# Optimization experiments

Measured on AMD Instinct MI355X. Metric: run time of the kernel, lower is better.

The kernel has to match this reference:

```python
import jax, jax.numpy as jnp
import numpy as np


def setup_inputs() -> dict:
    key = jax.random.key(0)
    k1, k2, k3, k4 = jax.random.split(key, 4)
    B, T, E, D = 4, 4096, 2048, 128
    x = jax.random.normal(k1, (B, T, E), dtype=jnp.float32)
    # nn.Linear(E, D, bias=False): y = x @ W where W is [E, D]
    scale = 1.0 / np.sqrt(E)
    Wq = jax.random.normal(k2, (E, D), dtype=jnp.float32) * scale
    Wk = jax.random.normal(k3, (E, D), dtype=jnp.float32) * scale
    Wv = jax.random.normal(k4, (E, D), dtype=jnp.float32) * scale
    return {"x": x, "Wq": Wq, "Wk": Wk, "Wv": Wv}


def reference(x, Wq, Wk, Wv):
    # Single attention head, prefill path (kv_cache=None, T_q == T_k).
    D = Wq.shape[1]
    Q = jnp.einsum('bte,ed->btd', x, Wq)
    K = jnp.einsum('bte,ed->btd', x, Wk)
    V = jnp.einsum('bte,ed->btd', x, Wv)
    scores = jnp.einsum('bqd,bkd->bqk', Q, K) / jnp.sqrt(jnp.float32(D))
    T = x.shape[1]
    causal = jnp.tril(jnp.ones((T, T), dtype=bool))  # [T_q, T_k]
    scores = jnp.where(causal[None, :, :], scores, -jnp.inf)
    attn = jax.nn.softmax(scores, axis=-1)
    out = jnp.einsum('bqk,bkd->bqd', attn, V)
    return out
```

## Files before the change

kernel.cpp:

```cpp
#include <hip/hip_runtime.h>
#include <hip/hip_bf16.h>

typedef short bf16x8 __attribute__((ext_vector_type(8)));
typedef float f32x4  __attribute__((ext_vector_type(4)));

#define T_SEQ 4096
#define NB    4
#define E_DIM 2048
#define D_DIM 128
#define M_TOT (NB * T_SEQ)
#define NCHUNK 4
#define CHUNK_KT 16
#define SM_SHIFT 12.0f

__device__ __forceinline__ ushort f2bf(float f) {
  union { float f; unsigned u; } c; c.f = f;
  unsigned u = c.u;
  unsigned r = (u + 0x7FFFu + ((u >> 16) & 1u)) >> 16;
  return (ushort)r;
}
__device__ __forceinline__ float bf2f(ushort u) {
  union { unsigned u; float f; } c; c.u = ((unsigned)u) << 16;
  return c.f;
}
__device__ __forceinline__ bf16x8 cvt8(const float4& lo, const float4& hi) {
  union { __hip_bfloat162 h; ushort u[2]; } t;
  union { ushort u[8]; bf16x8 v; } r;
  t.h = __float22bfloat162_rn(make_float2(lo.x, lo.y)); r.u[0] = t.u[0]; r.u[1] = t.u[1];
  t.h = __float22bfloat162_rn(make_float2(lo.z, lo.w)); r.u[2] = t.u[0]; r.u[3] = t.u[1];
  t.h = __float22bfloat162_rn(make_float2(hi.x, hi.y)); r.u[4] = t.u[0]; r.u[5] = t.u[1];
  t.h = __float22bfloat162_rn(make_float2(hi.z, hi.w)); r.u[6] = t.u[0]; r.u[7] = t.u[1];
  return r.v;
}

__device__ __forceinline__ void gl2lds16(const void* g, void* l) {
  __builtin_amdgcn_global_load_lds(
      (const __attribute__((address_space(1))) unsigned int*)g,
      (__attribute__((address_space(3))) unsigned int*)l, 16, 0, 0);
}

__global__ __launch_bounds__(256) void build_wt(const float* __restrict__ Wq,
                                                const float* __restrict__ Wk,
                                                const float* __restrict__ Wv,
                                                ushort* __restrict__ Wt) {
  __shared__ ushort tile[64][72];
  const int tid = threadIdx.x;
  const int k0 = blockIdx.x * 64, n0 = blockIdx.y * 64, o = blockIdx.z;
  const float* W = (o == 0) ? Wq : ((o == 1) ? Wk : Wv);
  for (int i = 0; i < 4; i++) {
    int c = tid + i * 256;
    int r = c >> 4, c4 = (c & 15) * 4;
    float4 v = *(const float4*)(W + (size_t)(k0 + r) * D_DIM + n0 + c4);
    ushort4 b4;
    b4.x = f2bf(v.x); b4.y = f2bf(v.y); b4.z = f2bf(v.z); b4.w = f2bf(v.w);
    *(ushort4*)(&tile[r][c4]) = b4;
  }
  __syncthreads();
  for (int i = 0; i < 2; i++) {
    int c = tid + i * 256;
    int nn = c >> 3, k8 = (c & 7) * 8;
    ushort tmp[8];
    for (int j = 0; j < 8; j++) tmp[j] = tile[k8 + j][nn];
    *(uint4*)(Wt + (size_t)((o << 7) + n0 + nn) * E_DIM + k0 + k8) = *(const uint4*)tmp;
  }
}

__global__ __launch_bounds__(256, 4) void qkv_gemm(const float* __restrict__ x,
                                                   const ushort* __restrict__ Wt,
                                                   ushort* __restrict__ Q,
                                                   ushort* __restrict__ K,
                                                   ushort* __restrict__ V) {
  __shared__ ushort As[2][64 * 64];
  __shared__ ushort Bs[2][96 * 64];

  const int tid  = threadIdx.x;
  const int wave = tid >> 6, lane = tid & 63;
  const int quad = lane >> 4, l16 = lane & 15;
  const int wm = wave >> 1, wn = wave & 1;
  const int m0 = blockIdx.x * 64;
  const int n0 = blockIdx.y * 96;

  f32x4 acc[2][3] = {};

  const int s_ = wave * 64 + lane;
  const int n_ = s_ >> 3, p_ = s_ & 7;

  const int ar_ = tid >> 2, aq4_ = tid & 3;
  const float* xrow = x + (size_t)(m0 + ar_) * E_DIM + aq4_ * 16;

#define DMA_B(k0_, buf_)                                                        \
  _Pragma("unroll")                                                             \
  for (int i_ = 0; i_ < 3; i_++) {                                              \
    int slotbase = i_ * 256 + wave * 64;                                        \
    int n = (i_ * 32) + n_;                           \
    int cg = p_ ^ (n & 7);                                                      \
    gl2lds16(Wt + (size_t)(n0 + n) * E_DIM + (k0_) + cg * 8,                    \
             (char*)(buf_) + (size_t)slotbase * 16);                            \
  }

#define GLOAD_A(k0_)                                                            \
  {                                                                             \
    const float* ap_ = xrow + (k0_);                                            \
    areg0 = *(const float4*)(ap_);                                              \
    areg1 = *(const float4*)(ap_ + 4);                                          \
    areg2 = *(const float4*)(ap_ + 8);                                          \
    areg3 = *(const float4*)(ap_ + 12);                                         \
  }

#define CVT_WRITE_A(bufidx)                                                     \
  {                                                                             \
    ushort* as_ = As[bufidx];                                                   \
    bf16x8 w0_ = cvt8(areg0, areg1);                                            \
    bf16x8 w1_ = cvt8(areg2, areg3);                                            \
    *(bf16x8*)(as_ + ar_ * 64 + (((aq4_ * 2)     ^ (ar_ & 7)) * 8)) = w0_;      \
    *(bf16x8*)(as_ + ar_ * 64 + (((aq4_ * 2 + 1) ^ (ar_ & 7)) * 8)) = w1_;      \
  }

#define COMPUTE(bufidx)                                                         \
  {                                                                             \
    const ushort* as_ = As[bufidx];                                             \
    const ushort* bs_ = Bs[bufidx];                                             \
    _Pragma("unroll")                                                           \
    for (int kk = 0; kk < 2; kk++) {                                            \
      const int slot = ((kk * 4 + quad) ^ (l16 & 7)) * 8;                       \
      bf16x8 af0 = *(const bf16x8*)(as_ + (wm * 32 + l16) * 64 + slot);         \
      bf16x8 af1 = *(const bf16x8*)(as_ + (wm * 32 + 16 + l16) * 64 + slot);    \
      _Pragma("unroll")                                                         \
      for (int ni = 0; ni < 3; ni++) {                                          \
        int n = wn * 48 + ni * 16 + l16;                                        \
        bf16x8 bf = *(const bf16x8*)(bs_ + n * 64 + slot);                      \
        acc[0][ni] = __builtin_amdgcn_mfma_f32_16x16x32_bf16(af0, bf, acc[0][ni], 0, 0, 0); \
        acc[1][ni] = __builtin_amdgcn_mfma_f32_16x16x32_bf16(af1, bf, acc[1][ni], 0, 0, 0); \
      }                                                                         \
    }                                                                           \
  }

  float4 areg0, areg1, areg2, areg3;

  GLOAD_A(0);
  DMA_B(0, Bs[0]);
  CVT_WRITE_A(0);
  __syncthreads();

  for (int it = 0; it < 32; it += 2) {
    GLOAD_A((it + 1) * 64);
    DMA_B((it + 1) * 64, Bs[1]);
    COMPUTE(0);
    CVT_WRITE_A(1);
    __syncthreads();
    if (it < 30) {
      GLOAD_A((it + 2) * 64);
      DMA_B((it + 2) * 64, Bs[0]);
      COMPUTE(1);
      CVT_WRITE_A(0);
      __syncthreads();
    } else {
      COMPUTE(1);
    }
  }

  for (int mi = 0; mi < 2; mi++)
    for (int ni = 0; ni < 3; ni++) {
      int colall = n0 + wn * 48 + ni * 16 + l16;
      int o = colall >> 7, d = colall & 127;
      ushort* dst = (o == 0) ? Q : ((o == 1) ? K : V);
      for (int r = 0; r < 4; r++) {
        int row = m0 + wm * 32 + mi * 16 + quad * 4 + r;
        dst[(size_t)row * D_DIM + d] = f2bf(acc[mi][ni][r]);
      }
    }
#undef DMA_B
#undef GLOAD_A
#undef CVT_WRITE_A
#undef COMPUTE
}

__global__ __launch_bounds__(256) void v_transpose(const ushort* __restrict__ V,
                                                   ushort* __restrict__ Vt) {
  __shared__ ushort tile[64][72];
  const int tid = threadIdx.x;
  const int t0 = blockIdx.x * 64, d0 = blockIdx.y * 64, b = blockIdx.z;
  for (int i = 0; i < 2; i++) {
    int c = tid + i * 256;
    int r = c >> 3, cc = (c & 7) * 8;
    *(uint4*)(&tile[r][cc]) = *(const uint4*)(V + (size_t)(b * T_SEQ + t0 + r) * D_DIM + d0 + cc);
  }
  __syncthreads();
  for (int i = 0; i < 2; i++) {
    int c = tid + i * 256;
    int dr = c >> 3, tc = (c & 7) * 8;
    ushort tmp[8];
    for (int j = 0; j < 8; j++) tmp[j] = tile[tc + j][dr];
    *(uint4*)(Vt + (size_t)(b * D_DIM + d0 + dr) * T_SEQ + t0 + tc) = *(const uint4*)tmp;
  }
}

__global__ __launch_bounds__(256) void attn_partial(const ushort* __restrict__ Q,
                                                    const ushort* __restrict__ K,
                                                    const ushort* __restrict__ Vt,
                                                    ushort* __restrict__ Po,
                                                    float* __restrict__ Ll) {
  const int qt = blockIdx.x, cq = blockIdx.y, b = blockIdx.z;
  const int kt0 = cq * CHUNK_KT;
  if (kt0 > qt) return;

  __shared__ ushort Kt[64][136];
  __shared__ ushort Vts[128][72];
  __shared__ ushort Pls[4][16][72];

  const int tid = threadIdx.x;
  const int wave = tid >> 6, lane = tid & 63;
  const int quad = lane >> 4, l16 = lane & 15;

  const int qrow = qt * 64 + wave * 16 + l16;
  bf16x8 qf[4];
  for (int kk = 0; kk < 4; kk++)
    qf[kk] = *(const bf16x8*)(Q + (size_t)(b * T_SEQ + qrow) * D_DIM + kk * 32 + quad * 8);

  bf16x8 ones;
  for (int j = 0; j < 8; j++) ones[j] = (short)0x3F80;

  f32x4 o_acc[8] = {};
  f32x4 lacc = {};
  const float scale2 = 0.08838834764831845f * 1.4426950408889634f;

  const int kt1 = min(qt, kt0 + CHUNK_KT - 1);

  for (int kt = kt0; kt <= kt1; kt++) {
    __syncthreads();
    for (int i = 0; i < 4; i++) {
      int c = tid + i * 256;
      int r = c >> 4, col = (c & 15) * 8;
      *(uint4*)(&Kt[r][col]) = *(const uint4*)(K + (size_t)(b * T_SEQ + kt * 64 + r) * D_DIM + col);
    }
    for (int i = 0; i < 4; i++) {
      int c = tid + i * 256;
      int dr = c >> 3, col = (c & 7) * 8;
      *(uint4*)(&Vts[dr][col]) = *(const uint4*)(Vt + (size_t)(b * D_DIM + dr) * T_SEQ + kt * 64 + col);
    }
    __syncthreads();

    f32x4 s[4] = {};
    for (int kk = 0; kk < 4; kk++) {
      const int kc = kk * 32 + quad * 8;
      for (int ni = 0; ni < 4; ni++) {
        bf16x8 bf = *(const bf16x8*)(&Kt[ni * 16 + l16][kc]);
        s[ni] = __builtin_amdgcn_mfma_f32_16x16x32_bf16(qf[kk], bf, s[ni], 0, 0, 0);
      }
    }
    if (kt == qt) {
      for (int ni = 0; ni < 4; ni++) {
        int kidx = kt * 64 + ni * 16 + l16;
        for (int r = 0; r < 4; r++) {
          int qidx = qt * 64 + wave * 16 + quad * 4 + r;
          float v = (kidx > qidx) ? -1e30f : (s[ni][r] * scale2 - SM_SHIFT);
          s[ni][r] = exp2f(v);
        }
      }
    } else {
      for (int ni = 0; ni < 4; ni++)
        for (int r = 0; r < 4; r++)
          s[ni][r] = exp2f(s[ni][r] * scale2 - SM_SHIFT);
    }
    for (int ni = 0; ni < 4; ni++)
      for (int r = 0; r < 4; r++)
        Pls[wave][quad * 4 + r][ni * 16 + l16] = f2bf(s[ni][r]);
    for (int kk2 = 0; kk2 < 2; kk2++) {
      const int kc = kk2 * 32 + quad * 8;
      bf16x8 pf = *(const bf16x8*)(&Pls[wave][l16][kc]);
      for (int ni = 0; ni < 8; ni++) {
        bf16x8 vf = *(const bf16x8*)(&Vts[ni * 16 + l16][kc]);
        o_acc[ni] = __builtin_amdgcn_mfma_f32_16x16x32_bf16(pf, vf, o_acc[ni], 0, 0, 0);
      }
      lacc = __builtin_amdgcn_mfma_f32_16x16x32_bf16(pf, ones, lacc, 0, 0, 0);
    }
  }

  const int slot = (b * 64 + qt) * NCHUNK + cq;
  for (int ni = 0; ni < 8; ni++)
    for (int r = 0; r < 4; r++) {
      int ql = wave * 16 + quad * 4 + r;
      Po[(size_t)slot * 8192 + ql * D_DIM + ni * 16 + l16] = f2bf(o_acc[ni][r]);
    }
  if (l16 == 0) {
    for (int r = 0; r < 4; r++) {
      int ql = wave * 16 + quad * 4 + r;
      Ll[slot * 64 + ql] = lacc[r];
    }
  }
}

__global__ __launch_bounds__(256) void attn_reduce(const ushort* __restrict__ Po,
                                                   const float* __restrict__ Ll,
                                                   float* __restrict__ out) {
  const int qt = blockIdx.x, b = blockIdx.y;
  const int nc = qt / CHUNK_KT + 1;
  const int tid = threadIdx.x;
  const int row = tid >> 2;
  const int c0  = (tid & 3) * 32;
  const int base_slot = (b * 64 + qt) * NCHUNK;

  float L = 0.f;
  for (int c = 0; c < nc; c++) L += Ll[(base_slot + c) * 64 + row];
  const float inv = 1.0f / L;

  const size_t orow = (size_t)(b * T_SEQ + qt * 64 + row) * D_DIM;
  for (int cc = 0; cc < 32; cc += 8) {
    float a[8] = {0,0,0,0,0,0,0,0};
    for (int c = 0; c < nc; c++) {
      const ushort* p = Po + (size_t)(base_slot + c) * 8192 + row * D_DIM + c0 + cc;
      ushort u[8];
      *(uint4*)u = *(const uint4*)p;
      for (int j = 0; j < 8; j++) a[j] += bf2f(u[j]);
    }
    float4 o0, o1;
    o0.x = a[0] * inv; o0.y = a[1] * inv; o0.z = a[2] * inv; o0.w = a[3] * inv;
    o1.x = a[4] * inv; o1.y = a[5] * inv; o1.z = a[6] * inv; o1.w = a[7] * inv;
    *(float4*)(out + orow + c0 + cc)     = o0;
    *(float4*)(out + orow + c0 + cc + 4) = o1;
  }
}

extern "C" void kernel_launch(void* const* d_in, const int* in_sizes, int n_in,
                              void* d_out, int out_size, void* d_ws, size_t ws_size,
                              hipStream_t stream) {
  const float* x  = (const float*)d_in[0];
  const float* Wq = (const float*)d_in[1];
  const float* Wk = (const float*)d_in[2];
  const float* Wv = (const float*)d_in[3];
  float* out = (float*)d_out;

  ushort* Q  = (ushort*)d_ws;
  ushort* Kb = Q  + (size_t)M_TOT * D_DIM;
  ushort* Vb = Kb + (size_t)M_TOT * D_DIM;
  ushort* Vt = Vb + (size_t)M_TOT * D_DIM;
  ushort* Wt = Vt + (size_t)M_TOT * D_DIM;
  ushort* Po = Wt + (size_t)384 * E_DIM;
  float*  Ll = (float*)(Po + (size_t)NB * 64 * NCHUNK * 8192);

  hipLaunchKernelGGL(build_wt,     dim3(32, 2, 3),       dim3(256), 0, stream, Wq, Wk, Wv, Wt);
  hipLaunchKernelGGL(qkv_gemm,     dim3(256, 4),         dim3(256), 0, stream, x, Wt, Q, Kb, Vb);
  hipLaunchKernelGGL(v_transpose,  dim3(64, 2, 4),       dim3(256), 0, stream, Vb, Vt);
  hipLaunchKernelGGL(attn_partial, dim3(64, NCHUNK, 4),  dim3(256), 0, stream, Q, Kb, Vt, Po, Ll);
  hipLaunchKernelGGL(attn_reduce,  dim3(64, 4),          dim3(256), 0, stream, Po, Ll, out);
}
```

Baseline: 297.7 us.

## Triple-buffer W tiles and prefetch two stages ahead in QKV GEMM

Moves the QKV projection GEMM from double buffering to a deeper pipeline. B tiles go into a rotating triple LDS buffer, and A is loaded from global two stages ahead using two register sets. Manual vmcnt/lgkmcnt waits and raw s_barrier replace __syncthreads, so the wait covers only the oldest outstanding DMA. This costs more LDS and registers, and the launch bound drops to 3 blocks per CU.

```diff
diff --git a/kernel.cpp b/kernel.cpp
--- a/kernel.cpp
+++ b/kernel.cpp
@@ -65,13 +65,13 @@
   }
 }
 
-__global__ __launch_bounds__(256, 4) void qkv_gemm(const float* __restrict__ x,
+__global__ __launch_bounds__(256, 3) void qkv_gemm(const float* __restrict__ x,
                                                    const ushort* __restrict__ Wt,
                                                    ushort* __restrict__ Q,
                                                    ushort* __restrict__ K,
                                                    ushort* __restrict__ V) {
   __shared__ ushort As[2][64 * 64];
-  __shared__ ushort Bs[2][96 * 64];
+  __shared__ ushort Bs[3][96 * 64];
 
   const int tid  = threadIdx.x;
   const int wave = tid >> 6, lane = tid & 63;
@@ -88,38 +88,38 @@
   const int ar_ = tid >> 2, aq4_ = tid & 3;
   const float* xrow = x + (size_t)(m0 + ar_) * E_DIM + aq4_ * 16;
 
-#define DMA_B(k0_, buf_)                                                        \
+#define DMA_B(k0_, dst_)                                                        \
   _Pragma("unroll")                                                             \
   for (int i_ = 0; i_ < 3; i_++) {                                              \
     int slotbase = i_ * 256 + wave * 64;                                        \
     int n = (i_ * 32) + n_;                           \
     int cg = p_ ^ (n & 7);                                                      \
     gl2lds16(Wt + (size_t)(n0 + n) * E_DIM + (k0_) + cg * 8,                    \
-             (char*)(buf_) + (size_t)slotbase * 16);                            \
-  }
-
-#define GLOAD_A(k0_)                                                            \
+             (char*)(dst_) + (size_t)slotbase * 16);                            \
+  }
+
+#define GLOAD_A(k0_, r0, r1, r2, r3)                                            \
   {                                                                             \
     const float* ap_ = xrow + (k0_);                                            \
-    areg0 = *(const float4*)(ap_);                                              \
-    areg1 = *(const float4*)(ap_ + 4);                                          \
-    areg2 = *(const float4*)(ap_ + 8);                                          \
-    areg3 = *(const float4*)(ap_ + 12);                                         \
-  }
-
-#define CVT_WRITE_A(bufidx)                                                     \
+    r0 = *(const float4*)(ap_);                                                 \
+    r1 = *(const float4*)(ap_ + 4);                                             \
+    r2 = *(const float4*)(ap_ + 8);                                             \
+    r3 = *(const float4*)(ap_ + 12);                                            \
+  }
+
+#define CVT_WRITE_A(dst_, r0, r1, r2, r3)                                       \
   {                                                                             \
-    ushort* as_ = As[bufidx];                                                   \
-    bf16x8 w0_ = cvt8(areg0, areg1);                                            \
-    bf16x8 w1_ = cvt8(areg2, areg3);                                            \
+    ushort* as_ = (dst_);                                                       \
+    bf16x8 w0_ = cvt8(r0, r1);                                                  \
+    bf16x8 w1_ = cvt8(r2, r3);                                                  \
     *(bf16x8*)(as_ + ar_ * 64 + (((aq4_ * 2)     ^ (ar_ & 7)) * 8)) = w0_;      \
     *(bf16x8*)(as_ + ar_ * 64 + (((aq4_ * 2 + 1) ^ (ar_ & 7)) * 8)) = w1_;      \
   }
 
-#define COMPUTE(bufidx)                                                         \
+#define COMPUTE(as_p, bs_p)                                                     \
   {                                                                             \
-    const ushort* as_ = As[bufidx];                                             \
-    const ushort* bs_ = Bs[bufidx];                                             \
+    const ushort* as_ = (as_p);                                                 \
+    const ushort* bs_ = (bs_p);                                                 \
     _Pragma("unroll")                                                           \
     for (int kk = 0; kk < 2; kk++) {                                            \
       const int slot = ((kk * 4 + quad) ^ (l16 & 7)) * 8;                       \
@@ -135,29 +135,50 @@
     }                                                                           \
   }
 
-  float4 areg0, areg1, areg2, areg3;
-
-  GLOAD_A(0);
+#define ROT_B() { ushort* t_ = bc; bc = bn1; bn1 = bn2; bn2 = t_; }
+
+  float4 sA0, sA1, sA2, sA3;
+  float4 sB0, sB1, sB2, sB3;
+
+  GLOAD_A(0, sA0, sA1, sA2, sA3);
   DMA_B(0, Bs[0]);
-  CVT_WRITE_A(0);
+  GLOAD_A(64, sB0, sB1, sB2, sB3);
+  DMA_B(64, Bs[1]);
+  CVT_WRITE_A(As[0], sA0, sA1, sA2, sA3);
   __syncthreads();
 
-  for (int it = 0; it < 32; it += 2) {
-    GLOAD_A((it + 1) * 64);
-    DMA_B((it + 1) * 64, Bs[1]);
-    COMPUTE(0);
-    CVT_WRITE_A(1);
-    __syncthreads();
-    if (it < 30) {
-      GLOAD_A((it + 2) * 64);
-      DMA_B((it + 2) * 64, Bs[0]);
-      COMPUTE(1);
-      CVT_WRITE_A(0);
-      __syncthreads();
-    } else {
-      COMPUTE(1);
-    }
-  }
+  ushort* bc  = Bs[0];
+  ushort* bn1 = Bs[1];
+  ushort* bn2 = Bs[2];
+
+  for (int it = 0; it < 30; it += 2) {
+    GLOAD_A((it + 2) * 64, sA0, sA1, sA2, sA3);
+    DMA_B((it + 2) * 64, bn2);
+    asm volatile("s_waitcnt vmcnt(14)" ::: "memory");
+    COMPUTE(As[0], bc);
+    CVT_WRITE_A(As[1], sB0, sB1, sB2, sB3);
+    asm volatile("s_waitcnt lgkmcnt(0)" ::: "memory");
+    __builtin_amdgcn_s_barrier();
+    __builtin_amdgcn_sched_barrier(0);
+    ROT_B();
+    GLOAD_A((it + 3) * 64, sB0, sB1, sB2, sB3);
+    DMA_B((it + 3) * 64, bn2);
+    asm volatile("s_waitcnt vmcnt(14)" ::: "memory");
+    COMPUTE(As[1], bc);
+    CVT_WRITE_A(As[0], sA0, sA1, sA2, sA3);
+    asm volatile("s_waitcnt lgkmcnt(0)" ::: "memory");
+    __builtin_amdgcn_s_barrier();
+    __builtin_amdgcn_sched_barrier(0);
+    ROT_B();
+  }
+  asm volatile("s_waitcnt vmcnt(7)" ::: "memory");
+  COMPUTE(As[0], bc);
+  CVT_WRITE_A(As[1], sB0, sB1, sB2, sB3);
+  asm volatile("s_waitcnt lgkmcnt(0)" ::: "memory");
+  __builtin_amdgcn_s_barrier();
+  ROT_B();
+  asm volatile("s_waitcnt vmcnt(0)" ::: "memory");
+  COMPUTE(As[1], bc);
 
   for (int mi = 0; mi < 2; mi++)
     for (int ni = 0; ni < 3; ni++) {
@@ -173,6 +194,7 @@
 #undef GLOAD_A
 #undef CVT_WRITE_A
 #undef COMPUTE
+#undef ROT_B
 }
 
 __global__ __launch_bounds__(256) void v_transpose(const ushort* __restrict__ V,
```

Measured after the change: 303.7 us. 1.02x slower.
